# Performance work log

Hardware: AMD Instinct MI355X
Metric: run time of the kernel (lower is better)

The kernel has to match this reference:

```python
import jax, jax.numpy as jnp
import numpy as np

E = 5          # number of experts / candidate encoders
NSUB = 13      # subband axis from x.reshape([B, 13, -1])


def _complex_corr_mean(y, y_):
    # y: [E, B, 13, F] (interleaved re/im), y_: [B, 13, F]
    ai, aj = y[..., 0::2], y[..., 1::2]        # [E,B,13,F/2]
    bi, bj = y_[..., 0::2], y_[..., 1::2]      # [B,13,F/2]
    i = (ai * bi + aj * bj).sum(-1)            # [E,B,13]
    j = (ai * bj - aj * bi).sum(-1)            # [E,B,13]
    c = i * i + j * j                          # |<a, conj(b)>|^2 per subband
    return c.mean(-1)                          # [E,B]


def setup_inputs() -> dict:
    key = jax.random.key(0)
    k = jax.random.split(key, 5)
    B, F, D = 4096, 9984, 512
    return {
        "x": jax.random.normal(k[0], (B, F), dtype=jnp.float32),
        "W_enc": jax.random.normal(k[1], (E, F, D), dtype=jnp.float32) * 0.02,
        "b_enc": jnp.zeros((E, D), dtype=jnp.float32),
        "W_dec": jax.random.normal(k[2], (E, D, F), dtype=jnp.float32) * 0.02,
        "b_dec": jnp.zeros((E, F), dtype=jnp.float32),
    }


def reference(x, W_enc, b_enc, W_dec, b_dec):
    B = x.shape[0]
    # per-expert encode: out[e] = encoder_e(x) -> latent code [E, B, D]
    out = jnp.einsum("bf,efd->ebd", x, W_enc) + b_enc[:, None, :]
    # per-expert decode: y[e] = decoder_e(out[e]) -> reconstruction [E, B, F]
    y = jnp.einsum("ebd,edf->ebf", out, W_dec) + b_dec[:, None, :]
    y = y.reshape(E, B, NSUB, -1)
    y_ = x.reshape(B, NSUB, -1)
    scores = _complex_corr_mean(y, y_)         # [E, B]
    idx = jnp.argmax(scores, axis=0)           # [B] best expert per sample
    # batch_gather: pick the winning expert's latent per sample
    sel = out[idx, jnp.arange(B)]              # [B, D]
    return sel
```

## Files before the change

kernel.cpp:

```cpp
#include <hip/hip_runtime.h>

#define E_ 5
#define B_ 4096
#define F_ 9984
#define D_ 512
#define NSUB_ 13
#define SUBW_ 768

typedef _Float16 f16;
typedef __attribute__((ext_vector_type(4))) _Float16 f16x4;
typedef __attribute__((ext_vector_type(8))) _Float16 f16x8;
typedef __attribute__((ext_vector_type(16))) float f32x16;

#define BK 32
#define PLANE_H 4096
#define BUF_H   16384

#define MFMA(a, b, c) __builtin_amdgcn_mfma_f32_32x32x16_f16((a), (b), (c), 0, 0, 0)

__device__ __forceinline__ void gload16(const f16* g, f16* l) {
    __builtin_amdgcn_global_load_lds(
        (const __attribute__((address_space(1))) void*)g,
        (__attribute__((address_space(3))) void*)l, 16, 0, 0);
}

__device__ __forceinline__ void computeK(const f16* L,
        int rA0, int kA0, int rA1, int kA1,
        int rB0, int kB0, int rB1, int kB1, int g,
        f32x16 accm[2][2], f32x16 accx[2][2]) {
    #pragma unroll
    for (int sub = 0; sub < 2; ++sub) {
        const int c = sub * 2 + g;
        f16x8 ah0 = *(const f16x8*)(L + 0*PLANE_H + rA0 + (((c ^ kA0)) << 3));
        f16x8 ah1 = *(const f16x8*)(L + 0*PLANE_H + rA1 + (((c ^ kA1)) << 3));
        f16x8 al0 = *(const f16x8*)(L + 1*PLANE_H + rA0 + (((c ^ kA0)) << 3));
        f16x8 al1 = *(const f16x8*)(L + 1*PLANE_H + rA1 + (((c ^ kA1)) << 3));
        f16x8 bh0 = *(const f16x8*)(L + 2*PLANE_H + rB0 + (((c ^ kB0)) << 3));
        f16x8 bh1 = *(const f16x8*)(L + 2*PLANE_H + rB1 + (((c ^ kB1)) << 3));
        f16x8 bl0 = *(const f16x8*)(L + 3*PLANE_H + rB0 + (((c ^ kB0)) << 3));
        f16x8 bl1 = *(const f16x8*)(L + 3*PLANE_H + rB1 + (((c ^ kB1)) << 3));
        accm[0][0] = MFMA(ah0, bh0, accm[0][0]);
        accm[0][1] = MFMA(ah0, bh1, accm[0][1]);
        accm[1][0] = MFMA(ah1, bh0, accm[1][0]);
        accm[1][1] = MFMA(ah1, bh1, accm[1][1]);
        accx[0][0] = MFMA(ah0, bl0, accx[0][0]);
        accx[0][0] = MFMA(al0, bh0, accx[0][0]);
        accx[0][1] = MFMA(ah0, bl1, accx[0][1]);
        accx[0][1] = MFMA(al0, bh1, accx[0][1]);
        accx[1][0] = MFMA(ah1, bl0, accx[1][0]);
        accx[1][0] = MFMA(al1, bh0, accx[1][0]);
        accx[1][1] = MFMA(ah1, bl1, accx[1][1]);
        accx[1][1] = MFMA(al1, bh1, accx[1][1]);
    }
}

__device__ __forceinline__ void gemm_core3(
    const f16* __restrict__ Ah, const f16* __restrict__ Al, int sA,
    const f16* __restrict__ Bh, const f16* __restrict__ Bl, int sB,
    int nk, f16* lds, int t, int wm, int wn, int l31, int g,
    f32x16 accm[2][2], f32x16 accx[2][2])
{
    const int lane = t & 63, wid = t >> 6;
    const int lrow = lane >> 2, lch = lane & 3;
    const f16* gp = (wid == 0) ? Ah : (wid == 1) ? Al : (wid == 2) ? Bh : Bl;
    const int gs = (wid < 2) ? sA : sB;
    f16* plane = lds + wid * PLANE_H;

    size_t goff[8];
    #pragma unroll
    for (int s = 0; s < 8; ++s) {
        const int row = s * 16 + lrow;
        goff[s] = (size_t)row * gs + ((lch ^ ((row >> 1) & 3)) << 3);
    }

    const int rowA0 = wm + l31,      rowA1 = wm + 32 + l31;
    const int rowB0 = wn + l31,      rowB1 = wn + 32 + l31;
    const int rA0 = rowA0 * BK, kA0 = (rowA0 >> 1) & 3;
    const int rA1 = rowA1 * BK, kA1 = (rowA1 >> 1) & 3;
    const int rB0 = rowB0 * BK, kB0 = (rowB0 >> 1) & 3;
    const int rB1 = rowB1 * BK, kB1 = (rowB1 >> 1) & 3;

    #pragma unroll
    for (int s = 0; s < 8; ++s)
        gload16(gp + goff[s], plane + s * (16 * BK));

    for (int kt = 0; kt < nk; ++kt) {
        const bool more = (kt + 1 < nk);
        if (more) {
            f16* dst = plane + ((kt + 1) & 1) * BUF_H;
            const int k0 = (kt + 1) * BK;
            #pragma unroll
            for (int s = 0; s < 8; ++s)
                gload16(gp + goff[s] + k0, dst + s * (16 * BK));
            asm volatile("s_waitcnt vmcnt(8)" ::: "memory");
        } else {
            asm volatile("s_waitcnt vmcnt(0)" ::: "memory");
        }
        __builtin_amdgcn_s_barrier();
        __builtin_amdgcn_sched_barrier(0);
        const f16* L = lds + (kt & 1) * BUF_H;
        __builtin_amdgcn_s_setprio(1);
        computeK(L, rA0, kA0, rA1, kA1, rB0, kB0, rB1, kB1, g, accm, accx);
        __builtin_amdgcn_s_setprio(0);
        __builtin_amdgcn_sched_barrier(0);
        __builtin_amdgcn_s_barrier();
        __builtin_amdgcn_sched_barrier(0);
    }
}

__global__ __launch_bounds__(256) void split_x(const float* __restrict__ x,
                                               f16* __restrict__ xhi, f16* __restrict__ xlo) {
    size_t i = ((size_t)blockIdx.x * 256 + threadIdx.x) * 4;
    float4 v = *(const float4*)&x[i];
    float vv[4] = {v.x, v.y, v.z, v.w};
    f16x4 h, l;
    #pragma unroll
    for (int k = 0; k < 4; ++k) {
        f16 hh = (f16)vv[k];
        h[k] = hh;
        l[k] = (f16)((vv[k] - (float)hh) * 2048.0f);
    }
    *(f16x4*)&xhi[i] = h;
    *(f16x4*)&xlo[i] = l;
}

__global__ __launch_bounds__(256) void splitT_W(const float* __restrict__ W,
                                                f16* __restrict__ Thi, f16* __restrict__ Tlo,
                                                int R, int C) {
    __shared__ float tile[64][65];
    const int rt = blockIdx.x, ct = blockIdx.y, e = blockIdx.z;
    const int t = threadIdx.x;
    const int r0 = rt * 64, c0 = ct * 64;
    const int tr = t >> 4, tc4 = (t & 15) * 4;
    const float* Wp = W + (size_t)e * R * C;
    #pragma unroll
    for (int p = 0; p < 4; ++p) {
        float4 v = *(const float4*)&Wp[(size_t)(r0 + tr + p*16) * C + c0 + tc4];
        tile[tr + p*16][tc4 + 0] = v.x;
        tile[tr + p*16][tc4 + 1] = v.y;
        tile[tr + p*16][tc4 + 2] = v.z;
        tile[tr + p*16][tc4 + 3] = v.w;
    }
    __syncthreads();
    f16* Th = Thi + (size_t)e * R * C;
    f16* Tl = Tlo + (size_t)e * R * C;
    #pragma unroll
    for (int p = 0; p < 4; ++p) {
        const int cr = tr + p*16;
        f16x4 h, l;
        #pragma unroll
        for (int k = 0; k < 4; ++k) {
            float v = tile[tc4 + k][cr] * 64.0f;
            f16 hh = (f16)v;
            h[k] = hh;
            l[k] = (f16)((v - (float)hh) * 2048.0f);
        }
        size_t off = (size_t)(c0 + cr) * R + r0 + tc4;
        *(f16x4*)&Th[off] = h;
        *(f16x4*)&Tl[off] = l;
    }
}

__global__ __launch_bounds__(256, 2) void mm_enc2(
    const f16* __restrict__ xhi, const f16* __restrict__ xlo,
    const f16* __restrict__ wthi, const f16* __restrict__ wtlo,
    const float* __restrict__ bias, int Kloc,
    f16* __restrict__ outHi, f16* __restrict__ outLo)
{
    __shared__ f16 lds[2 * BUF_H];
    const int gx = blockIdx.x;
    const int de = gx % 20;
    const int bl = gx / 20;
    const int bt = blockIdx.y * 4 + bl;
    const int ks = blockIdx.z;
    const int dt = de & 3, e = de >> 2;
    const int koff = ks * Kloc;
    const int t = threadIdx.x, lane = t & 63, l31 = lane & 31, g = lane >> 5, wid = t >> 6;
    const int wm = (wid >> 1) * 64, wn = (wid & 1) * 64;
    const f16* Ah = xhi + (size_t)bt * 128 * F_ + koff;
    const f16* Al = xlo + (size_t)bt * 128 * F_ + koff;
    const f16* Bh = wthi + ((size_t)e * D_ + dt * 128) * F_ + koff;
    const f16* Bl = wtlo + ((size_t)e * D_ + dt * 128) * F_ + koff;
    f32x16 accm[2][2] = {}, accx[2][2] = {};
    gemm_core3(Ah, Al, F_, Bh, Bl, F_, Kloc / BK, lds, t, wm, wn, l31, g, accm, accx);

    f16* oH = outHi + (size_t)ks * E_ * B_ * D_;
    f16* oL = outLo + (size_t)ks * E_ * B_ * D_;
    #pragma unroll
    for (int fn = 0; fn < 2; ++fn) {
        const int d = dt * 128 + wn + fn * 32 + l31;
        const float be = bias ? bias[e * D_ + d] : 0.0f;
        #pragma unroll
        for (int fm = 0; fm < 2; ++fm) {
            #pragma unroll
            for (int r = 0; r < 16; ++r) {
                float v = (accm[fm][fn][r] + accx[fm][fn][r] * (1.0f/2048.0f)) * (1.0f/64.0f) + be;
                int brow = bt * 128 + wm + fm * 32 + (r & 3) + 8 * (r >> 2) + 4 * g;
                size_t off = ((size_t)e * B_ + brow) * D_ + d;
                f16 h = (f16)v;
                oH[off] = h;
                oL[off] = (f16)((v - (float)h) * 2048.0f);
            }
        }
    }
}

__global__ __launch_bounds__(256) void combine_k(
    const f16* __restrict__ pH, const f16* __restrict__ pL,
    const float* __restrict__ b_enc,
    f16* __restrict__ oH, f16* __restrict__ oL)
{
    const size_t NP = (size_t)E_ * B_ * D_;
    size_t i = ((size_t)blockIdx.x * 256 + threadIdx.x) * 8;
    f16x8 h0 = *(const f16x8*)(pH + i);
    f16x8 l0 = *(const f16x8*)(pL + i);
    f16x8 h1 = *(const f16x8*)(pH + NP + i);
    f16x8 l1 = *(const f16x8*)(pL + NP + i);
    const int d = (int)(i % D_);
    const int e = (int)(i / ((size_t)B_ * D_));
    f16x8 oh, ol;
    #pragma unroll
    for (int k = 0; k < 8; ++k) {
        float v = (float)h0[k] + (float)l0[k] * (1.0f/2048.0f)
                + (float)h1[k] + (float)l1[k] * (1.0f/2048.0f)
                + b_enc[e * D_ + d + k];
        f16 hh = (f16)v;
        oh[k] = hh;
        ol[k] = (f16)((v - (float)hh) * 2048.0f);
    }
    *(f16x8*)&oH[i] = oh;
    *(f16x8*)&oL[i] = ol;
}

__global__ __launch_bounds__(256, 2) void mm_dec2(
    const f16* __restrict__ wthi, const f16* __restrict__ wtlo,
    const f16* __restrict__ ohi, const f16* __restrict__ olo,
    const float* __restrict__ b_dec, const float* __restrict__ x,
    float* __restrict__ ijbuf)
{
    __shared__ f16 lds[2 * BUF_H];
    const int bt = blockIdx.x;
    const int ft = blockIdx.y;
    const int se = blockIdx.z;
    const int e = se % 5, s = se / 5;
    const int t = threadIdx.x, lane = t & 63, l31 = lane & 31, g = lane >> 5, wid = t >> 6;
    const int wm = (wid >> 1) * 64, wn = (wid & 1) * 64;
    const int f0blk = s * SUBW_ + ft * 128;
    const f16* Ah = wthi + ((size_t)e * F_ + f0blk) * D_;
    const f16* Al = wtlo + ((size_t)e * F_ + f0blk) * D_;
    const f16* Bh = ohi + ((size_t)e * B_ + bt * 128) * D_;
    const f16* Bl = olo + ((size_t)e * B_ + bt * 128) * D_;
    f32x16 accm[2][2] = {}, accx[2][2] = {};
    gemm_core3(Ah, Al, D_, Bh, Bl, D_, D_ / BK, lds, t, wm, wn, l31, g, accm, accx);

    float ia[2] = {0.f, 0.f}, ja[2] = {0.f, 0.f};
    #pragma unroll
    for (int fm = 0; fm < 2; ++fm) {
        #pragma unroll
        for (int q = 0; q < 8; ++q) {
            const int r = q * 2;
            const int fg = f0blk + wm + fm * 32 + (r & 3) + 8 * (r >> 2) + 4 * g;
            const float2 bd = *(const float2*)&b_dec[(size_t)e * F_ + fg];
            #pragma unroll
            for (int fn = 0; fn < 2; ++fn) {
                const int b = bt * 128 + wn + fn * 32 + l31;
                const float2 xv = *(const float2*)&x[(size_t)b * F_ + fg];
                float y0 = (accm[fm][fn][r]     + accx[fm][fn][r]     * (1.0f/2048.0f)) * (1.0f/64.0f) + bd.x;
                float y1 = (accm[fm][fn][r + 1] + accx[fm][fn][r + 1] * (1.0f/2048.0f)) * (1.0f/64.0f) + bd.y;
                ia[fn] += y0 * xv.x + y1 * xv.y;
                ja[fn] += y0 * xv.y - y1 * xv.x;
            }
        }
    }
    #pragma unroll
    for (int fn = 0; fn < 2; ++fn) {
        ia[fn] += __shfl_xor(ia[fn], 32, 64);
        ja[fn] += __shfl_xor(ja[fn], 32, 64);
    }
    float* red = (float*)lds;
    const int wr = wid >> 1, wc = wid & 1;
    if (wr == 0 && lane < 32) {
        #pragma unroll
        for (int fn = 0; fn < 2; ++fn) {
            red[(wc * 64 + fn * 32 + l31) * 2 + 0] = ia[fn];
            red[(wc * 64 + fn * 32 + l31) * 2 + 1] = ja[fn];
        }
    }
    __syncthreads();
    if (wr == 1 && lane < 32) {
        #pragma unroll
        for (int fn = 0; fn < 2; ++fn) {
            float gi = ia[fn] + red[(wc * 64 + fn * 32 + l31) * 2 + 0];
            float gj = ja[fn] + red[(wc * 64 + fn * 32 + l31) * 2 + 1];
            int b = bt * 128 + wc * 64 + fn * 32 + l31;
            size_t base = (((size_t)(e * NSUB_ + s)) * 6 + ft) * 2;
            ijbuf[(base + 0) * B_ + b] = gi;
            ijbuf[(base + 1) * B_ + b] = gj;
        }
    }
}

__global__ __launch_bounds__(256) void argmax2(const float* __restrict__ ijbuf, int* __restrict__ idx) {
    int b = blockIdx.x * 256 + threadIdx.x;
    float best = -1.0f; int bi = 0;
    for (int e = 0; e < E_; ++e) {
        float sc = 0.f;
        for (int s = 0; s < NSUB_; ++s) {
            float ii = 0.f, jj = 0.f;
            #pragma unroll
            for (int ft = 0; ft < 6; ++ft) {
                size_t base = (((size_t)(e * NSUB_ + s)) * 6 + ft) * 2;
                ii += ijbuf[base * B_ + b];
                jj += ijbuf[(base + 1) * B_ + b];
            }
            sc += ii * ii + jj * jj;
        }
        if (sc > best) { best = sc; bi = e; }
    }
    idx[b] = bi;
}

__global__ __launch_bounds__(256) void gather2(const f16* __restrict__ outHi, const f16* __restrict__ outLo,
                                               const int* __restrict__ idx, float* __restrict__ sel) {
    int tg = blockIdx.x * 256 + threadIdx.x;
    int b = tg >> 7, dq = (tg & 127) * 4;
    int e = idx[b];
    size_t off = ((size_t)e * B_ + b) * D_ + dq;
    f16x4 h = *(const f16x4*)&outHi[off];
    f16x4 l = *(const f16x4*)&outLo[off];
    float4 o;
    o.x = (float)h[0] + (float)l[0] * (1.0f/2048.0f);
    o.y = (float)h[1] + (float)l[1] * (1.0f/2048.0f);
    o.z = (float)h[2] + (float)l[2] * (1.0f/2048.0f);
    o.w = (float)h[3] + (float)l[3] * (1.0f/2048.0f);
    *(float4*)&sel[(size_t)b * D_ + dq] = o;
}

__global__ __launch_bounds__(256) void enc_gemm(const float* __restrict__ x,
                                                const float* __restrict__ W_enc,
                                                const float* __restrict__ b_enc,
                                                float* __restrict__ out)
{
    __shared__ float As[16][68];
    __shared__ float Bs[16][68];
    const int btile = blockIdx.x;
    const int en    = blockIdx.y;
    const int e  = en >> 3;
    const int n0 = (en & 7) * 64;
    const int b0 = btile * 64;
    const int tid = threadIdx.x;
    const int tx = tid & 15, ty = tid >> 4;
    const float* Wp = W_enc + (size_t)e * F_ * D_;
    const int arow = tid >> 2;
    const int ac4  = (tid & 3) * 4;
    const int bk   = tid >> 4;
    const int bn   = (tid & 15) * 4;
    float acc[4][4] = {};
    for (int k0 = 0; k0 < F_; k0 += 16) {
        float4 av = *(const float4*)&x[(size_t)(b0 + arow) * F_ + k0 + ac4];
        As[ac4 + 0][arow] = av.x; As[ac4 + 1][arow] = av.y;
        As[ac4 + 2][arow] = av.z; As[ac4 + 3][arow] = av.w;
        float4 bv = *(const float4*)&Wp[(size_t)(k0 + bk) * D_ + n0 + bn];
        *(float4*)&Bs[bk][bn] = bv;
        __syncthreads();
        #pragma unroll
        for (int k = 0; k < 16; ++k) {
            float4 a = *(const float4*)&As[k][ty * 4];
            float4 b = *(const float4*)&Bs[k][tx * 4];
            float ar[4] = {a.x, a.y, a.z, a.w};
            float br[4] = {b.x, b.y, b.z, b.w};
            #pragma unroll
            for (int r = 0; r < 4; ++r)
                #pragma unroll
                for (int c = 0; c < 4; ++c)
                    acc[r][c] += ar[r] * br[c];
        }
        __syncthreads();
    }
    float4 be = *(const float4*)&b_enc[e * D_ + n0 + tx * 4];
    #pragma unroll
    for (int r = 0; r < 4; ++r) {
        int b = b0 + ty * 4 + r;
        float4 o;
        o.x = acc[r][0] + be.x; o.y = acc[r][1] + be.y;
        o.z = acc[r][2] + be.z; o.w = acc[r][3] + be.w;
        *(float4*)&out[((size_t)e * B_ + b) * D_ + n0 + tx * 4] = o;
    }
}

__global__ __launch_bounds__(256) void dec_score(const float* __restrict__ out,
                                                 const float* __restrict__ W_dec,
                                                 const float* __restrict__ b_dec,
                                                 const float* __restrict__ x,
                                                 float* __restrict__ cbuf)
{
    __shared__ float As[16][68];
    __shared__ float Bs[16][68];
    const int btile = blockIdx.x;
    const int es    = blockIdx.y;
    const int e = es / 13;
    const int s = es % 13;
    const int b0 = btile * 64;
    const int fbase = s * SUBW_;
    const int tid = threadIdx.x;
    const int tx = tid & 15, ty = tid >> 4;
    const float* Ap = out   + (size_t)e * B_ * D_;
    const float* Wp = W_dec + (size_t)e * D_ * F_;
    const int arow = tid >> 2;
    const int ac4  = (tid & 3) * 4;
    const int bk   = tid >> 4;
    const int bn   = (tid & 15) * 4;
    float ip[4] = {}, jp[4] = {};
    for (int u = 0; u < 12; ++u) {
        const int f0 = fbase + u * 64;
        float acc[4][4] = {};
        for (int k0 = 0; k0 < D_; k0 += 16) {
            float4 av = *(const float4*)&Ap[(size_t)(b0 + arow) * D_ + k0 + ac4];
            As[ac4 + 0][arow] = av.x; As[ac4 + 1][arow] = av.y;
            As[ac4 + 2][arow] = av.z; As[ac4 + 3][arow] = av.w;
            float4 bv = *(const float4*)&Wp[(size_t)(k0 + bk) * F_ + f0 + bn];
            *(float4*)&Bs[bk][bn] = bv;
            __syncthreads();
            #pragma unroll
            for (int k = 0; k < 16; ++k) {
                float4 a = *(const float4*)&As[k][ty * 4];
                float4 b = *(const float4*)&Bs[k][tx * 4];
                float ar[4] = {a.x, a.y, a.z, a.w};
                float br[4] = {b.x, b.y, b.z, b.w};
                #pragma unroll
                for (int r = 0; r < 4; ++r)
                    #pragma unroll
                    for (int c = 0; c < 4; ++c)
                        acc[r][c] += ar[r] * br[c];
            }
            __syncthreads();
        }
        float4 bd = *(const float4*)&b_dec[(size_t)e * F_ + f0 + tx * 4];
        #pragma unroll
        for (int r = 0; r < 4; ++r) {
            int b = b0 + ty * 4 + r;
            float4 xv = *(const float4*)&x[(size_t)b * F_ + f0 + tx * 4];
            float y0 = acc[r][0] + bd.x;
            float y1 = acc[r][1] + bd.y;
            float y2 = acc[r][2] + bd.z;
            float y3 = acc[r][3] + bd.w;
            ip[r] += y0 * xv.x + y1 * xv.y + y2 * xv.z + y3 * xv.w;
            jp[r] += y0 * xv.y - y1 * xv.x + y2 * xv.w - y3 * xv.z;
        }
    }
    #pragma unroll
    for (int r = 0; r < 4; ++r) {
        float iv = ip[r], jv = jp[r];
        #pragma unroll
        for (int m = 1; m < 16; m <<= 1) {
            iv += __shfl_xor(iv, m, 64);
            jv += __shfl_xor(jv, m, 64);
        }
        if (tx == 0) {
            int b = b0 + ty * 4 + r;
            cbuf[((size_t)e * B_ + b) * NSUB_ + s] = iv * iv + jv * jv;
        }
    }
}

__global__ __launch_bounds__(256) void argmax_k(const float* __restrict__ cbuf,
                                                int* __restrict__ idx)
{
    int b = blockIdx.x * blockDim.x + threadIdx.x;
    if (b >= B_) return;
    float best = -1e30f;
    int bi = 0;
    for (int e = 0; e < E_; ++e) {
        float ssum = 0.f;
        #pragma unroll
        for (int s = 0; s < NSUB_; ++s)
            ssum += cbuf[((size_t)e * B_ + b) * NSUB_ + s];
        if (ssum > best) { best = ssum; bi = e; }
    }
    idx[b] = bi;
}

__global__ __launch_bounds__(256) void gather_k(const float* __restrict__ out,
                                                const int* __restrict__ idx,
                                                float* __restrict__ sel)
{
    int t = blockIdx.x * blockDim.x + threadIdx.x;
    int b = t >> 7;
    int c = (t & 127) * 4;
    int e = idx[b];
    *(float4*)&sel[(size_t)b * D_ + c] =
        *(const float4*)&out[((size_t)e * B_ + b) * D_ + c];
}

extern "C" void kernel_launch(void* const* d_in, const int* in_sizes, int n_in,
                              void* d_out, int out_size, void* d_ws, size_t ws_size,
                              hipStream_t stream)
{
    const float* x     = (const float*)d_in[0];
    const float* W_enc = (const float*)d_in[1];
    const float* b_enc = (const float*)d_in[2];
    const float* W_dec = (const float*)d_in[3];
    const float* b_dec = (const float*)d_in[4];
    float* sel = (float*)d_out;

    const size_t szXplane = (size_t)B_ * F_ * sizeof(f16);
    const size_t szWplane = (size_t)E_ * F_ * D_ * sizeof(f16);
    const size_t szOplane = (size_t)E_ * B_ * D_ * sizeof(f16);
    const size_t szIJ     = (size_t)E_ * NSUB_ * 6 * 2 * B_ * sizeof(float);
    const size_t need      = 2*szXplane + 2*szWplane + 2*szOplane + szIJ + (size_t)B_*4;
    const size_t needSplit = need + 4*szOplane;

    if (ws_size >= need) {
        char* p = (char*)d_ws;
        f16* xhi  = (f16*)p; p += szXplane;
        f16* xlo  = (f16*)p; p += szXplane;
        f16* wthi = (f16*)p; p += szWplane;
        f16* wtlo = (f16*)p; p += szWplane;
        f16* ohi  = (f16*)p; p += szOplane;
        f16* olo  = (f16*)p; p += szOplane;
        float* ij = (float*)p; p += szIJ;
        int* idx  = (int*)p; p += (size_t)B_*4;

        split_x<<<39936, 256, 0, stream>>>(x, xhi, xlo);
        splitT_W<<<dim3(F_/64, D_/64, E_), 256, 0, stream>>>(W_enc, wthi, wtlo, F_, D_);

        if (ws_size >= needSplit) {
            f16* pH = (f16*)p; p += 2*szOplane;
            f16* pL = (f16*)p;
            mm_enc2<<<dim3(80, 8, 2), 256, 0, stream>>>(xhi, xlo, wthi, wtlo,
                                                        nullptr, F_/2, pH, pL);
            combine_k<<<(E_*B_*D_)/(8*256), 256, 0, stream>>>(pH, pL, b_enc, ohi, olo);
        } else {
            mm_enc2<<<dim3(80, 8, 1), 256, 0, stream>>>(xhi, xlo, wthi, wtlo,
                                                        b_enc, F_, ohi, olo);
        }
        splitT_W<<<dim3(D_/64, F_/64, E_), 256, 0, stream>>>(W_dec, wthi, wtlo, D_, F_);
        mm_dec2<<<dim3(32, 6, 65), 256, 0, stream>>>(wthi, wtlo, ohi, olo, b_dec, x, ij);
        argmax2<<<16, 256, 0, stream>>>(ij, idx);
        gather2<<<2048, 256, 0, stream>>>(ohi, olo, idx, sel);
    } else {
        float* out  = (float*)d_ws;
        float* cbuf = out + (size_t)E_ * B_ * D_;
        int*   idx  = (int*)(cbuf + (size_t)E_ * B_ * NSUB_);
        enc_gemm <<<dim3(64, 40), 256, 0, stream>>>(x, W_enc, b_enc, out);
        dec_score<<<dim3(64, 65), 256, 0, stream>>>(out, W_dec, b_dec, x, cbuf);
        argmax_k <<<dim3(B_ / 256), 256, 0, stream>>>(cbuf, idx);
        gather_k <<<dim3(B_ * D_ / 4 / 256), 256, 0, stream>>>(out, idx, sel);
    }
}
```

Measured before the change: 1.725 ms.

## Unroll GEMM k-loop by two with constant LDS offsets and stage x tile in LDS

The shared GEMM core is unrolled by two so each double-buffer half uses a compile-time LDS offset. Swizzled read addresses and global pointers are precomputed and bumped incrementally, which removes per-iteration address arithmetic. The decoder epilogue now loads its 128x128 slice of x with coalesced float4 reads into a padded LDS tile and reads it back from there. The old path did strided per-lane float2 global loads. This adds an extra barrier and enlarges the decoder's LDS footprint, which may reduce occupancy. The unrolled loop also assumes an even number of k tiles.

```diff
diff --git a/kernel.cpp b/kernel.cpp
--- a/kernel.cpp
+++ b/kernel.cpp
@@ -24,21 +24,25 @@
         (__attribute__((address_space(3))) void*)l, 16, 0, 0);
 }
 
-__device__ __forceinline__ void computeK(const f16* L,
-        int rA0, int kA0, int rA1, int kA1,
-        int rB0, int kB0, int rB1, int kB1, int g,
+template<int BOFF>
+__device__ __forceinline__ void computeK5(const f16* lds,
+        int aA0s0, int aA0s1, int aA1s0, int aA1s1,
+        int aB0s0, int aB0s1, int aB1s0, int aB1s1,
         f32x16 accm[2][2], f32x16 accx[2][2]) {
     #pragma unroll
     for (int sub = 0; sub < 2; ++sub) {
-        const int c = sub * 2 + g;
-        f16x8 ah0 = *(const f16x8*)(L + 0*PLANE_H + rA0 + (((c ^ kA0)) << 3));
-        f16x8 ah1 = *(const f16x8*)(L + 0*PLANE_H + rA1 + (((c ^ kA1)) << 3));
-        f16x8 al0 = *(const f16x8*)(L + 1*PLANE_H + rA0 + (((c ^ kA0)) << 3));
-        f16x8 al1 = *(const f16x8*)(L + 1*PLANE_H + rA1 + (((c ^ kA1)) << 3));
-        f16x8 bh0 = *(const f16x8*)(L + 2*PLANE_H + rB0 + (((c ^ kB0)) << 3));
-        f16x8 bh1 = *(const f16x8*)(L + 2*PLANE_H + rB1 + (((c ^ kB1)) << 3));
-        f16x8 bl0 = *(const f16x8*)(L + 3*PLANE_H + rB0 + (((c ^ kB0)) << 3));
-        f16x8 bl1 = *(const f16x8*)(L + 3*PLANE_H + rB1 + (((c ^ kB1)) << 3));
+        const int oA0 = sub ? aA0s1 : aA0s0;
+        const int oA1 = sub ? aA1s1 : aA1s0;
+        const int oB0 = sub ? aB0s1 : aB0s0;
+        const int oB1 = sub ? aB1s1 : aB1s0;
+        f16x8 ah0 = *(const f16x8*)(lds + BOFF + 0*PLANE_H + oA0);
+        f16x8 ah1 = *(const f16x8*)(lds + BOFF + 0*PLANE_H + oA1);
+        f16x8 al0 = *(const f16x8*)(lds + BOFF + 1*PLANE_H + oA0);
+        f16x8 al1 = *(const f16x8*)(lds + BOFF + 1*PLANE_H + oA1);
+        f16x8 bh0 = *(const f16x8*)(lds + BOFF + 2*PLANE_H + oB0);
+        f16x8 bh1 = *(const f16x8*)(lds + BOFF + 2*PLANE_H + oB1);
+        f16x8 bl0 = *(const f16x8*)(lds + BOFF + 3*PLANE_H + oB0);
+        f16x8 bl1 = *(const f16x8*)(lds + BOFF + 3*PLANE_H + oB1);
         accm[0][0] = MFMA(ah0, bh0, accm[0][0]);
         accm[0][1] = MFMA(ah0, bh1, accm[0][1]);
         accm[1][0] = MFMA(ah1, bh0, accm[1][0]);
@@ -54,7 +58,7 @@
     }
 }
 
-__device__ __forceinline__ void gemm_core3(
+__device__ __forceinline__ void gemm_core5(
     const f16* __restrict__ Ah, const f16* __restrict__ Al, int sA,
     const f16* __restrict__ Bh, const f16* __restrict__ Bl, int sB,
     int nk, f16* lds, int t, int wm, int wn, int l31, int g,
@@ -64,43 +68,70 @@
     const int lrow = lane >> 2, lch = lane & 3;
     const f16* gp = (wid == 0) ? Ah : (wid == 1) ? Al : (wid == 2) ? Bh : Bl;
     const int gs = (wid < 2) ? sA : sB;
-    f16* plane = lds + wid * PLANE_H;
-
-    size_t goff[8];
+
+    const f16* gps[8];
+    int ldoff[8];
     #pragma unroll
     for (int s = 0; s < 8; ++s) {
         const int row = s * 16 + lrow;
-        goff[s] = (size_t)row * gs + ((lch ^ ((row >> 1) & 3)) << 3);
+        gps[s] = gp + (size_t)row * gs + ((lch ^ ((row >> 1) & 3)) << 3);
+        ldoff[s] = wid * PLANE_H + s * (16 * BK);
     }
 
     const int rowA0 = wm + l31,      rowA1 = wm + 32 + l31;
     const int rowB0 = wn + l31,      rowB1 = wn + 32 + l31;
-    const int rA0 = rowA0 * BK, kA0 = (rowA0 >> 1) & 3;
-    const int rA1 = rowA1 * BK, kA1 = (rowA1 >> 1) & 3;
-    const int rB0 = rowB0 * BK, kB0 = (rowB0 >> 1) & 3;
-    const int rB1 = rowB1 * BK, kB1 = (rowB1 >> 1) & 3;
+    const int kA0 = (rowA0 >> 1) & 3, kA1 = (rowA1 >> 1) & 3;
+    const int kB0 = (rowB0 >> 1) & 3, kB1 = (rowB1 >> 1) & 3;
+    const int aA0s0 = rowA0 * BK + (((0 + g) ^ kA0) << 3);
+    const int aA0s1 = rowA0 * BK + (((2 + g) ^ kA0) << 3);
+    const int aA1s0 = rowA1 * BK + (((0 + g) ^ kA1) << 3);
+    const int aA1s1 = rowA1 * BK + (((2 + g) ^ kA1) << 3);
+    const int aB0s0 = rowB0 * BK + (((0 + g) ^ kB0) << 3);
+    const int aB0s1 = rowB0 * BK + (((2 + g) ^ kB0) << 3);
+    const int aB1s0 = rowB1 * BK + (((0 + g) ^ kB1) << 3);
+    const int aB1s1 = rowB1 * BK + (((2 + g) ^ kB1) << 3);
 
     #pragma unroll
     for (int s = 0; s < 8; ++s)
-        gload16(gp + goff[s], plane + s * (16 * BK));
-
-    for (int kt = 0; kt < nk; ++kt) {
-        const bool more = (kt + 1 < nk);
-        if (more) {
-            f16* dst = plane + ((kt + 1) & 1) * BUF_H;
-            const int k0 = (kt + 1) * BK;
+        gload16(gps[s], lds + ldoff[s]);
+    #pragma unroll
+    for (int s = 0; s < 8; ++s)
+        gps[s] += BK;
+
+    for (int kt = 0; kt < nk; kt += 2) {
+        #pragma unroll
+        for (int s = 0; s < 8; ++s)
+            gload16(gps[s], lds + BUF_H + ldoff[s]);
+        #pragma unroll
+        for (int s = 0; s < 8; ++s)
+            gps[s] += BK;
+        asm volatile("s_waitcnt vmcnt(8)" ::: "memory");
+        __builtin_amdgcn_s_barrier();
+        __builtin_amdgcn_sched_barrier(0);
+        __builtin_amdgcn_s_setprio(1);
+        computeK5<0>(lds, aA0s0, aA0s1, aA1s0, aA1s1,
+                     aB0s0, aB0s1, aB1s0, aB1s1, accm, accx);
+        __builtin_amdgcn_s_setprio(0);
+        __builtin_amdgcn_sched_barrier(0);
+        __builtin_amdgcn_s_barrier();
+        __builtin_amdgcn_sched_barrier(0);
+
+        if (kt + 2 < nk) {
             #pragma unroll
             for (int s = 0; s < 8; ++s)
-                gload16(gp + goff[s] + k0, dst + s * (16 * BK));
+                gload16(gps[s], lds + ldoff[s]);
+            #pragma unroll
+            for (int s = 0; s < 8; ++s)
+                gps[s] += BK;
             asm volatile("s_waitcnt vmcnt(8)" ::: "memory");
         } else {
             asm volatile("s_waitcnt vmcnt(0)" ::: "memory");
         }
         __builtin_amdgcn_s_barrier();
         __builtin_amdgcn_sched_barrier(0);
-        const f16* L = lds + (kt & 1) * BUF_H;
         __builtin_amdgcn_s_setprio(1);
-        computeK(L, rA0, kA0, rA1, kA1, rB0, kB0, rB1, kB1, g, accm, accx);
+        computeK5<BUF_H>(lds, aA0s0, aA0s1, aA1s0, aA1s1,
+                         aB0s0, aB0s1, aB1s0, aB1s1, accm, accx);
         __builtin_amdgcn_s_setprio(0);
         __builtin_amdgcn_sched_barrier(0);
         __builtin_amdgcn_s_barrier();
@@ -182,7 +213,7 @@
     const f16* Bh = wthi + ((size_t)e * D_ + dt * 128) * F_ + koff;
     const f16* Bl = wtlo + ((size_t)e * D_ + dt * 128) * F_ + koff;
     f32x16 accm[2][2] = {}, accx[2][2] = {};
-    gemm_core3(Ah, Al, F_, Bh, Bl, F_, Kloc / BK, lds, t, wm, wn, l31, g, accm, accx);
+    gemm_core5(Ah, Al, F_, Bh, Bl, F_, Kloc / BK, lds, t, wm, wn, l31, g, accm, accx);
 
     f16* oH = outHi + (size_t)ks * E_ * B_ * D_;
     f16* oL = outLo + (size_t)ks * E_ * B_ * D_;
@@ -238,7 +269,7 @@
     const float* __restrict__ b_dec, const float* __restrict__ x,
     float* __restrict__ ijbuf)
 {
-    __shared__ f16 lds[2 * BUF_H];
+    __shared__ __align__(16) f16 lds[33280];
     const int bt = blockIdx.x;
     const int ft = blockIdx.y;
     const int se = blockIdx.z;
@@ -251,24 +282,43 @@
     const f16* Bh = ohi + ((size_t)e * B_ + bt * 128) * D_;
     const f16* Bl = olo + ((size_t)e * B_ + bt * 128) * D_;
     f32x16 accm[2][2] = {}, accx[2][2] = {};
-    gemm_core3(Ah, Al, D_, Bh, Bl, D_, D_ / BK, lds, t, wm, wn, l31, g, accm, accx);
-
+    gemm_core5(Ah, Al, D_, Bh, Bl, D_, D_ / BK, lds, t, wm, wn, l31, g, accm, accx);
+
+    float* xs = (float*)lds;
+    {
+        const int fb = (t & 31) * 4;
+        const int h  = fb >> 6, fl = fb & 63;
+        float* dst0 = xs + h * (128 * 65) + fl;
+        const float* src = &x[(size_t)(bt * 128 + (t >> 5)) * F_ + f0blk + fb];
+        #pragma unroll
+        for (int it = 0; it < 16; ++it) {
+            const int b = (t >> 5) + it * 8;
+            float4 v = *(const float4*)(src + (size_t)it * 8 * F_);
+            float* dst = dst0 + b * 65;
+            dst[0] = v.x; dst[1] = v.y; dst[2] = v.z; dst[3] = v.w;
+        }
+    }
+    __syncthreads();
+
+    const float* xsw = xs + (wm >> 6) * (128 * 65);
     float ia[2] = {0.f, 0.f}, ja[2] = {0.f, 0.f};
     #pragma unroll
     for (int fm = 0; fm < 2; ++fm) {
         #pragma unroll
         for (int q = 0; q < 8; ++q) {
             const int r = q * 2;
-            const int fg = f0blk + wm + fm * 32 + (r & 3) + 8 * (r >> 2) + 4 * g;
+            const int fl = fm * 32 + (r & 3) + 8 * (r >> 2) + 4 * g;
+            const int fg = f0blk + wm + fl;
             const float2 bd = *(const float2*)&b_dec[(size_t)e * F_ + fg];
             #pragma unroll
             for (int fn = 0; fn < 2; ++fn) {
-                const int b = bt * 128 + wn + fn * 32 + l31;
-                const float2 xv = *(const float2*)&x[(size_t)b * F_ + fg];
+                const int bl_ = wn + fn * 32 + l31;
+                const float x0 = xsw[bl_ * 65 + fl];
+                const float x1 = xsw[bl_ * 65 + fl + 1];
                 float y0 = (accm[fm][fn][r]     + accx[fm][fn][r]     * (1.0f/2048.0f)) * (1.0f/64.0f) + bd.x;
                 float y1 = (accm[fm][fn][r + 1] + accx[fm][fn][r + 1] * (1.0f/2048.0f)) * (1.0f/64.0f) + bd.y;
-                ia[fn] += y0 * xv.x + y1 * xv.y;
-                ja[fn] += y0 * xv.y - y1 * xv.x;
+                ia[fn] += y0 * x0 + y1 * x1;
+                ja[fn] += y0 * x1 - y1 * x0;
             }
         }
     }
@@ -277,6 +327,7 @@
         ia[fn] += __shfl_xor(ia[fn], 32, 64);
         ja[fn] += __shfl_xor(ja[fn], 32, 64);
     }
+    __syncthreads();
     float* red = (float*)lds;
     const int wr = wid >> 1, wc = wid & 1;
     if (wr == 0 && lane < 32) {
```

Result: no change. 1.709 ms (-0.9%).
